# Kernel tuning notes

Measured on AMD Instinct MI355X. Metric: run time of the kernel, lower is better.

The kernel has to match this reference:

```python
import jax, jax.numpy as jnp
import numpy as np

NUM_HEADS = 16


def setup_inputs() -> dict:
    key = jax.random.key(0)
    ks = jax.random.split(key, 9)
    B, N, C, R, T = 16, 1024, 1024, 64, 10
    s = 0.02
    x = jax.random.normal(ks[0], (B, N, C), dtype=jnp.float32)
    W_qkv = jax.random.normal(ks[1], (3 * C, C), dtype=jnp.float32) * s
    W_proj = jax.random.normal(ks[2], (C, C), dtype=jnp.float32) * s
    b_proj = jax.random.normal(ks[3], (C,), dtype=jnp.float32) * s
    A_k = jax.random.normal(ks[4], (T, R, C), dtype=jnp.float32) * s
    B_k = jax.random.normal(ks[5], (T, C, R), dtype=jnp.float32) * s
    A_v = jax.random.normal(ks[6], (T, R, C), dtype=jnp.float32) * s
    B_v = jax.random.normal(ks[7], (T, C, R), dtype=jnp.float32) * s
    return {"x": x, "W_qkv": W_qkv, "W_proj": W_proj, "b_proj": b_proj,
            "A_k": A_k, "B_k": B_k, "A_v": A_v, "B_v": B_v, "task": 4}


def reference(x, W_qkv, W_proj, b_proj, A_k, B_k, A_v, B_v, task):
    B, N, C = x.shape
    H = NUM_HEADS
    hd = C // H
    scale = hd ** (-0.5)

    # qkv projection: x @ W_qkv.T -> [B,N,3C] -> [3,B,H,N,hd]
    qkv = (x @ W_qkv.T).reshape(B, N, 3, H, hd).transpose(2, 0, 3, 1, 4)
    q, k, v = qkv[0], qkv[1], qkv[2]

    # merged LoRA weights: sum_{t<=task} B[t] @ A[t] -> [C, C]
    w_k = jnp.einsum('tcr,trd->cd', B_k[:task + 1], A_k[:task + 1])
    w_v = jnp.einsum('tcr,trd->cd', B_v[:task + 1], A_v[:task + 1])
    # F.linear(x, W) = x @ W.T ; reshape to [B,H,N,hd]
    dk = (x @ w_k.T).reshape(B, N, H, hd).transpose(0, 2, 1, 3)
    dv = (x @ w_v.T).reshape(B, N, H, hd).transpose(0, 2, 1, 3)
    k = k + dk
    v = v + dv

    attn = jax.nn.softmax(jnp.einsum('bhnd,bhmd->bhnm', q, k) * scale, axis=-1)
    out = jnp.einsum('bhnm,bhmd->bhnd', attn, v)
    out = out.transpose(0, 2, 1, 3).reshape(B, N, C)
    return out @ W_proj.T + b_proj
```

## Files before the change

kernel.cpp:

```cpp
#include <hip/hip_runtime.h>

typedef __attribute__((ext_vector_type(4))) float f32x4;
typedef __attribute__((ext_vector_type(8))) short s16x8;
typedef __attribute__((ext_vector_type(2))) unsigned int u32x2;
typedef __attribute__((ext_vector_type(4))) unsigned int u32x4;

#define LOG2E 1.44269504088896340736f

__device__ inline unsigned short f2b(float f) {
  unsigned int u = __float_as_uint(f);
  unsigned int r = (u + 0x7FFFu + ((u >> 16) & 1u)) >> 16;
  return (unsigned short)r;
}

__device__ inline unsigned int cvtpk_bf16(float lo, float hi) {
  unsigned int r;
  asm("v_cvt_pk_bf16_f32 %0, %1, %2" : "=v"(r) : "v"(lo), "v"(hi));
  return r;
}

__device__ inline void gload_lds16(const unsigned short* g, unsigned short* l) {
  __builtin_amdgcn_global_load_lds(
      (const __attribute__((address_space(1))) unsigned int*)g,
      (__attribute__((address_space(3))) unsigned int*)l, 16, 0, 0);
}

__global__ __launch_bounds__(256) void lora_merge(const float* __restrict__ A_k,
                                                  const float* __restrict__ B_k,
                                                  const float* __restrict__ A_v,
                                                  const float* __restrict__ B_v,
                                                  float* __restrict__ wk,
                                                  float* __restrict__ wv,
                                                  const int* __restrict__ taskp) {
  const float* A_ = blockIdx.y ? A_v : A_k;
  const float* B_ = blockIdx.y ? B_v : B_k;
  float* Wd = blockIdx.y ? wv : wk;
  __shared__ float Bs[64][65];
  __shared__ float As[64][65];
  const int tile = blockIdx.x;
  const int c0 = (tile >> 4) * 64, d0 = (tile & 15) * 64;
  const int tid = threadIdx.x;
  const int tx = tid & 15, ty = tid >> 4;
  const int T = *taskp + 1;
  float acc[4][4] = {};
  const int r = tid >> 2, cb = (tid & 3) * 16;
  for (int t = 0; t < T; ++t) {
    __syncthreads();
    const float* srcB = B_ + (size_t)t * 65536 + (size_t)(c0 + r) * 64 + cb;
    const float* srcA = A_ + (size_t)t * 65536 + (size_t)r * 1024 + d0 + cb;
#pragma unroll
    for (int j = 0; j < 16; j += 4) {
      f32x4 vb = *(const f32x4*)(srcB + j);
      Bs[r][cb + j] = vb.x; Bs[r][cb + j + 1] = vb.y;
      Bs[r][cb + j + 2] = vb.z; Bs[r][cb + j + 3] = vb.w;
      f32x4 va = *(const f32x4*)(srcA + j);
      As[r][cb + j] = va.x; As[r][cb + j + 1] = va.y;
      As[r][cb + j + 2] = va.z; As[r][cb + j + 3] = va.w;
    }
    __syncthreads();
#pragma unroll 8
    for (int rr = 0; rr < 64; ++rr) {
      float bv[4], av[4];
#pragma unroll
      for (int i = 0; i < 4; ++i) bv[i] = Bs[ty * 4 + i][rr];
#pragma unroll
      for (int j = 0; j < 4; ++j) av[j] = As[rr][tx * 4 + j];
#pragma unroll
      for (int i = 0; i < 4; ++i)
#pragma unroll
        for (int j = 0; j < 4; ++j) acc[i][j] += bv[i] * av[j];
    }
  }
#pragma unroll
  for (int i = 0; i < 4; ++i)
#pragma unroll
    for (int j = 0; j < 4; ++j)
      Wd[(size_t)(c0 + ty * 4 + i) * 1024 + d0 + tx * 4 + j] = acc[i][j];
}

__global__ void prep_cvt(const float* __restrict__ x, const float* __restrict__ Wproj,
                         unsigned short* __restrict__ xb, unsigned short* __restrict__ Wp) {
  int i = blockIdx.x * 256 + threadIdx.x;
  const float* src;
  unsigned short* dst;
  int idx;
  if (i < 4194304) { src = x; dst = xb; idx = i; }
  else { idx = i - 4194304; if (idx >= 262144) return; src = Wproj; dst = Wp; }
  f32x4 v = ((const f32x4*)src)[idx];
  unsigned short o0 = f2b(v.x), o1 = f2b(v.y), o2 = f2b(v.z), o3 = f2b(v.w);
  unsigned long long pack = (unsigned long long)o0 | ((unsigned long long)o1 << 16) |
                            ((unsigned long long)o2 << 32) | ((unsigned long long)o3 << 48);
  ((unsigned long long*)dst)[idx] = pack;
}

__global__ void build_wc(const float* __restrict__ Wqkv, const float* __restrict__ wk,
                         const float* __restrict__ wv, unsigned short* __restrict__ Wc) {
  int i = blockIdx.x * 256 + threadIdx.x;
  int e = i * 4;
  f32x4 v = *(const f32x4*)(Wqkv + e);
  int row = e >> 10;
  if (row >= 2048) {
    f32x4 d = *(const f32x4*)(wv + (e - 2097152));
    v = v + d;
  } else if (row >= 1024) {
    f32x4 d = *(const f32x4*)(wk + (e - 1048576));
    v = v + d;
  }
  unsigned short o0 = f2b(v.x), o1 = f2b(v.y), o2 = f2b(v.z), o3 = f2b(v.w);
  unsigned long long pack = (unsigned long long)o0 | ((unsigned long long)o1 << 16) |
                            ((unsigned long long)o2 << 32) | ((unsigned long long)o3 << 48);
  ((unsigned long long*)Wc)[i] = pack;
}

template <int OUT_BF16, int ADD_BIAS>
__global__ __launch_bounds__(512, 1) void gemm256(const unsigned short* __restrict__ A,
                                                  const unsigned short* __restrict__ B,
                                                  void* __restrict__ Cout,
                                                  const float* __restrict__ bias,
                                                  int M, int N, int K) {
  __shared__ unsigned short SA[4][8192];
  __shared__ unsigned short SB[4][8192];
  const int tid = threadIdx.x;
  const int w = tid >> 6, l = tid & 63;
  const int lr = l & 15, lg = l >> 4;
  const int wm = w >> 2, wn = w & 3;

  const int lin = blockIdx.y * gridDim.x + blockIdx.x;
  const int cpx = (gridDim.x * gridDim.y) >> 3;
  const int s = (lin & 7) * cpx + (lin >> 3);
  const int bx = s % gridDim.x, by = s / gridDim.x;

  const int cs = tid ^ (((tid >> 5) & 1) << 1);
  const int r_st = ((cs >> 6) << 4) | ((cs >> 2) & 15);
  const int k_st = (cs & 3) << 3;
  const unsigned short* gA0 = A + (size_t)(by * 256 + r_st) * K + k_st;
  const unsigned short* gA1 = A + (size_t)(by * 256 + 128 + r_st) * K + k_st;
  const unsigned short* gB0 = B + (size_t)(bx * 256 + r_st) * K + k_st;
  const unsigned short* gB1 = B + (size_t)(bx * 256 + 128 + r_st) * K + k_st;
  const int wb = w * 512;

  const int swz = ((lr >> 3) & 1) << 4;
  const int fbase = lr * 32 + lg * 8;
  const int hA = wm * 4096;
  const int hB = (wn >> 1) * 4096;
  const int nb = (wn & 1) * 4;

  f32x4 acc[8][4] = {};
  const int NT = K >> 5;

#pragma unroll
  for (int t = 0; t < 3; ++t) {
    gload_lds16(gA0 + t * 32, &SA[t][wb]);
    gload_lds16(gA1 + t * 32, &SA[t][4096 + wb]);
    gload_lds16(gB0 + t * 32, &SB[t][wb]);
    gload_lds16(gB1 + t * 32, &SB[t][4096 + wb]);
  }
  asm volatile("s_waitcnt vmcnt(8)" ::: "memory");
  __builtin_amdgcn_s_barrier();
  __builtin_amdgcn_sched_barrier(0);

  for (int t = 0; t < NT; ++t) {
    const int slot = t & 3;
    const int ts = (t + 3 < NT) ? (t + 3) : (NT - 1);
    const int ssl = (t + 3) & 3;
    const unsigned short* sa = &SA[slot][hA];
    const unsigned short* sb = &SB[slot][hB];
    s16x8 af[8], bf[2];
#pragma unroll
    for (int m = 0; m < 8; ++m)
      af[m] = *(const s16x8*)&sa[(m * 512 + fbase) ^ swz];
#pragma unroll
    for (int n = 0; n < 2; ++n)
      bf[n] = *(const s16x8*)&sb[((nb + n) * 512 + fbase) ^ swz];
    gload_lds16(gA0 + ts * 32, &SA[ssl][wb]);
    gload_lds16(gA1 + ts * 32, &SA[ssl][4096 + wb]);
    __builtin_amdgcn_s_barrier();
    asm volatile("s_waitcnt lgkmcnt(0)" ::: "memory");
    __builtin_amdgcn_sched_barrier(0);
    __builtin_amdgcn_s_setprio(1);
#pragma unroll
    for (int m = 0; m < 8; ++m)
#pragma unroll
      for (int n = 0; n < 2; ++n)
        acc[m][n] = __builtin_amdgcn_mfma_f32_16x16x32_bf16(af[m], bf[n], acc[m][n], 0, 0, 0);
    __builtin_amdgcn_s_setprio(0);
    __builtin_amdgcn_sched_barrier(0);
    __builtin_amdgcn_s_barrier();
#pragma unroll
    for (int n = 0; n < 2; ++n)
      bf[n] = *(const s16x8*)&sb[((nb + 2 + n) * 512 + fbase) ^ swz];
    gload_lds16(gB0 + ts * 32, &SB[ssl][wb]);
    gload_lds16(gB1 + ts * 32, &SB[ssl][4096 + wb]);
    __builtin_amdgcn_s_barrier();
    asm volatile("s_waitcnt lgkmcnt(0)" ::: "memory");
    __builtin_amdgcn_sched_barrier(0);
    __builtin_amdgcn_s_setprio(1);
#pragma unroll
    for (int m = 0; m < 8; ++m)
#pragma unroll
      for (int n = 0; n < 2; ++n)
        acc[m][2 + n] = __builtin_amdgcn_mfma_f32_16x16x32_bf16(af[m], bf[n], acc[m][2 + n], 0, 0, 0);
    __builtin_amdgcn_s_setprio(0);
    __builtin_amdgcn_sched_barrier(0);
    asm volatile("s_waitcnt vmcnt(8)" ::: "memory");
    __builtin_amdgcn_s_barrier();
    __builtin_amdgcn_sched_barrier(0);
  }

  const int crow0 = by * 256 + wm * 128;
  const int ccol0 = bx * 256 + wn * 64;
  if (OUT_BF16) {
    unsigned short* C = (unsigned short*)Cout;
#pragma unroll
    for (int m = 0; m < 8; ++m)
#pragma unroll
      for (int n = 0; n < 4; ++n)
#pragma unroll
        for (int rr = 0; rr < 4; ++rr) {
          int row = crow0 + m * 16 + lg * 4 + rr;
          int col = ccol0 + n * 16 + lr;
          C[(size_t)row * N + col] = f2b(acc[m][n][rr]);
        }
  } else {
    float* C = (float*)Cout;
#pragma unroll
    for (int m = 0; m < 8; ++m)
#pragma unroll
      for (int n = 0; n < 4; ++n)
#pragma unroll
        for (int rr = 0; rr < 4; ++rr) {
          int row = crow0 + m * 16 + lg * 4 + rr;
          int col = ccol0 + n * 16 + lr;
          float b = ADD_BIAS ? bias[col] : 0.f;
          C[(size_t)row * N + col] = acc[m][n][rr] + b;
        }
  }
}

__global__ __launch_bounds__(64) void transpose_v(const unsigned short* __restrict__ qkv,
                                                  unsigned short* __restrict__ vT) {
  __shared__ unsigned short T[64 * 65];
  const int bh = blockIdx.x >> 4;
  const int nt = blockIdx.x & 15;
  const int b = bh >> 4, h = bh & 15;
  const int l = threadIdx.x;
  const unsigned short* src = qkv + (size_t)(b * 1024 + nt * 64) * 3072 + 2048 + h * 64;
#pragma unroll
  for (int p = 0; p < 8; ++p) {
    int slot = p * 64 + l;
    int n = slot >> 3, dc = (slot & 7) * 8;
    u32x4 v = *(const u32x4*)(src + (size_t)n * 3072 + dc);
    const unsigned short* vs = (const unsigned short*)&v;
#pragma unroll
    for (int j = 0; j < 8; ++j) T[n * 65 + dc + j] = vs[j];
  }
  __syncthreads();
  unsigned short* dst = vT + (size_t)bh * 65536 + nt * 64;
#pragma unroll
  for (int p = 0; p < 8; ++p) {
    int slot = p * 64 + l;
    int d = slot >> 3, nc = (slot & 7) * 8;
    union { unsigned short s[8]; u32x4 v; } tmp;
#pragma unroll
    for (int j = 0; j < 8; ++j) tmp.s[j] = T[(nc + j) * 65 + d];
    *(u32x4*)(dst + (size_t)d * 1024 + nc) = tmp.v;
  }
}

__global__ __launch_bounds__(512) void attn_fwd(const unsigned short* __restrict__ qkv,
                                                const unsigned short* __restrict__ vT,
                                                unsigned short* __restrict__ out) {
  const int tid = threadIdx.x;
  const int w = tid >> 6, l = tid & 63;
  const int lr = l & 15, lg = l >> 4;
  const int bid = blockIdx.x;
  const int g = (bid & 7) * 32 + (bid >> 5);
  const int qt2 = (bid >> 3) & 3;
  const int b = g >> 4, h = g & 15;

  __shared__ unsigned short Ks[2][4096];
  __shared__ unsigned short Vs[2][4096];
  __shared__ unsigned int Ps[16][576];

  const size_t base = (size_t)b * 1024 * 3072 + h * 64;
  const unsigned short* Qp = qkv + base;
  const unsigned short* Kp = qkv + base + 1024;
  const unsigned short* vTp = vT + (size_t)(b * 16 + h) * 65536;

  const float SSCALE = 0.125f * LOG2E;
  const int qb = qt2 * 256;
  s16x8 qf[2][2];
#pragma unroll
  for (int qg = 0; qg < 2; ++qg) {
    const int qrow = qb + qg * 128 + w * 16 + lr;
    qf[qg][0] = *(const s16x8*)(Qp + (size_t)qrow * 3072 + lg * 8);
    qf[qg][1] = *(const s16x8*)(Qp + (size_t)qrow * 3072 + 32 + lg * 8);
#pragma unroll
    for (int kk = 0; kk < 2; ++kk)
#pragma unroll
      for (int j = 0; j < 8; ++j) {
        float f = __uint_as_float(((unsigned int)(unsigned short)qf[qg][kk][j]) << 16) * SSCALE;
        qf[qg][kk][j] = (short)f2b(f);
      }
  }

  f32x4 o[2][4] = {};
  float lrun[2] = {0.f, 0.f};

  const int srow = tid >> 3;
  const int csrc = (tid & 7) ^ (srow & 7);

  gload_lds16(Kp + (size_t)srow * 3072 + csrc * 8, &Ks[0][w * 512]);
  gload_lds16(vTp + (size_t)srow * 1024 + csrc * 8, &Vs[0][w * 512]);
  __syncthreads();

  for (int t = 0; t < 16; ++t) {
    const int cur = t & 1;
    if (t < 15) {
      const int kv1 = (t + 1) * 64;
      gload_lds16(Kp + (size_t)(kv1 + srow) * 3072 + csrc * 8, &Ks[cur ^ 1][w * 512]);
      gload_lds16(vTp + (size_t)srow * 1024 + kv1 + csrc * 8, &Vs[cur ^ 1][w * 512]);
    }
    const unsigned short* Kb = &Ks[cur][0];
    const unsigned short* Vb = &Vs[cur][0];

#pragma unroll
    for (int qg = 0; qg < 2; ++qg) {
      unsigned int* Pw = &Ps[(w << 1) | qg][0];
      f32x4 sc[4];
#pragma unroll
      for (int tt = 0; tt < 4; ++tt) {
        f32x4 a = {0.f, 0.f, 0.f, 0.f};
#pragma unroll
        for (int kk = 0; kk < 2; ++kk) {
          int krow = tt * 16 + lr;
          s16x8 kf = *(const s16x8*)&Kb[krow * 64 + ((((kk * 32 + lg * 8) >> 3) ^ (krow & 7)) << 3)];
          a = __builtin_amdgcn_mfma_f32_16x16x32_bf16(kf, qf[qg][kk], a, 0, 0, 0);
        }
        sc[tt] = a;
      }

#pragma unroll
      for (int tt = 0; tt < 4; ++tt) {
        float p0 = exp2f(sc[tt][0]);
        float p1 = exp2f(sc[tt][1]);
        float p2 = exp2f(sc[tt][2]);
        float p3 = exp2f(sc[tt][3]);
        lrun[qg] += (p0 + p1) + (p2 + p3);
        u32x2 pk;
        pk.x = cvtpk_bf16(p0, p1);
        pk.y = cvtpk_bf16(p2, p3);
        *(u32x2*)&Pw[lr * 36 + tt * 8 + lg * 2] = pk;
      }
      __builtin_amdgcn_sched_barrier(0);

#pragma unroll
      for (int kk = 0; kk < 2; ++kk) {
        u32x4 pu = *(const u32x4*)&Pw[lr * 36 + kk * 16 + lg * 4];
        s16x8 pf = __builtin_bit_cast(s16x8, pu);
#pragma unroll
        for (int dt = 0; dt < 4; ++dt) {
          int vrow = dt * 16 + lr;
          s16x8 vf = *(const s16x8*)&Vb[vrow * 64 + ((((kk * 32 + lg * 8) >> 3) ^ (vrow & 7)) << 3)];
          o[qg][dt] = __builtin_amdgcn_mfma_f32_16x16x32_bf16(pf, vf, o[qg][dt], 0, 0, 0);
        }
      }
    }
    __syncthreads();
  }

#pragma unroll
  for (int qg = 0; qg < 2; ++qg) {
    float lr2 = lrun[qg];
    lr2 += __shfl_xor(lr2, 16);
    lr2 += __shfl_xor(lr2, 32);
    float lq[4];
#pragma unroll
    for (int rr = 0; rr < 4; ++rr) lq[rr] = 1.f / __shfl(lr2, lg * 4 + rr);
    const size_t orow0 = (size_t)b * 1024 + qb + qg * 128 + w * 16;
#pragma unroll
    for (int dt = 0; dt < 4; ++dt)
#pragma unroll
      for (int rr = 0; rr < 4; ++rr)
        out[(orow0 + lg * 4 + rr) * 1024 + h * 64 + dt * 16 + lr] = f2b(o[qg][dt][rr] * lq[rr]);
  }
}

extern "C" void kernel_launch(void* const* d_in, const int* in_sizes, int n_in,
                              void* d_out, int out_size, void* d_ws, size_t ws_size,
                              hipStream_t stream) {
  const float* x = (const float*)d_in[0];
  const float* Wqkv = (const float*)d_in[1];
  const float* Wproj = (const float*)d_in[2];
  const float* bproj = (const float*)d_in[3];
  const float* A_k = (const float*)d_in[4];
  const float* B_k = (const float*)d_in[5];
  const float* A_v = (const float*)d_in[6];
  const float* B_v = (const float*)d_in[7];
  const int* task = (const int*)d_in[8];

  char* ws = (char*)d_ws;
  float* wk = (float*)ws;
  float* wv = (float*)(ws + (4ull << 20));
  unsigned short* xb = (unsigned short*)(ws + (8ull << 20));
  unsigned short* Wc = (unsigned short*)(ws + (40ull << 20));
  unsigned short* Wp = (unsigned short*)(ws + (46ull << 20));
  unsigned short* qkv = (unsigned short*)(ws + (48ull << 20));
  unsigned short* ao = (unsigned short*)(ws + (144ull << 20));
  unsigned short* vT = xb;

  lora_merge<<<dim3(256, 2), 256, 0, stream>>>(A_k, B_k, A_v, B_v, wk, wv, task);
  prep_cvt<<<17408, 256, 0, stream>>>(x, Wproj, xb, Wp);
  build_wc<<<3072, 256, 0, stream>>>(Wqkv, wk, wv, Wc);
  gemm256<1, 0><<<dim3(12, 64), 512, 0, stream>>>(xb, Wc, qkv, nullptr, 16384, 3072, 1024);
  transpose_v<<<4096, 64, 0, stream>>>(qkv, vT);
  attn_fwd<<<1024, 512, 0, stream>>>(qkv, vT, ao);
  gemm256<0, 1><<<dim3(4, 64), 512, 0, stream>>>(ao, Wp, d_out, bproj, 16384, 1024, 1024);
}
```

Before: 341.3 us.

## Interleave both query groups' MFMAs and compute softmax row sums via MFMA with ones

The attention inner loop now computes QK^T scores for both query groups together and shares each K fragment load between them. It writes both P tiles before a single PV phase that also shares V fragment loads. The running softmax denominator no longer comes from VALU adds and shuffles; it is accumulated by an extra MFMA of P against a vector of bf16 ones, which sums the bf16-rounded probabilities. s_setprio hints are added around MFMA blocks to favour matrix issue. The cost is more live registers for the doubled score accumulators, plus two extra MFMAs per kk step.

```diff
diff --git a/kernel.cpp b/kernel.cpp
--- a/kernel.cpp
+++ b/kernel.cpp
@@ -304,8 +304,12 @@
       }
   }
 
+  s16x8 ONES;
+#pragma unroll
+  for (int j = 0; j < 8; ++j) ONES[j] = (short)0x3F80;
+
   f32x4 o[2][4] = {};
-  float lrun[2] = {0.f, 0.f};
+  f32x4 o4[2] = {};
 
   const int srow = tid >> 3;
   const int csrc = (tid & 7) ^ (srow & 7);
@@ -324,59 +328,62 @@
     const unsigned short* Kb = &Ks[cur][0];
     const unsigned short* Vb = &Vs[cur][0];
 
+    f32x4 sc[2][4] = {};
+    __builtin_amdgcn_s_setprio(1);
+#pragma unroll
+    for (int kk = 0; kk < 2; ++kk)
+#pragma unroll
+      for (int tt = 0; tt < 4; ++tt) {
+        int krow = tt * 16 + lr;
+        s16x8 kf = *(const s16x8*)&Kb[krow * 64 + ((((kk * 32 + lg * 8) >> 3) ^ (krow & 7)) << 3)];
+        sc[0][tt] = __builtin_amdgcn_mfma_f32_16x16x32_bf16(kf, qf[0][kk], sc[0][tt], 0, 0, 0);
+        sc[1][tt] = __builtin_amdgcn_mfma_f32_16x16x32_bf16(kf, qf[1][kk], sc[1][tt], 0, 0, 0);
+      }
+    __builtin_amdgcn_s_setprio(0);
+
 #pragma unroll
     for (int qg = 0; qg < 2; ++qg) {
       unsigned int* Pw = &Ps[(w << 1) | qg][0];
-      f32x4 sc[4];
 #pragma unroll
       for (int tt = 0; tt < 4; ++tt) {
-        f32x4 a = {0.f, 0.f, 0.f, 0.f};
-#pragma unroll
-        for (int kk = 0; kk < 2; ++kk) {
-          int krow = tt * 16 + lr;
-          s16x8 kf = *(const s16x8*)&Kb[krow * 64 + ((((kk * 32 + lg * 8) >> 3) ^ (krow & 7)) << 3)];
-          a = __builtin_amdgcn_mfma_f32_16x16x32_bf16(kf, qf[qg][kk], a, 0, 0, 0);
-        }
-        sc[tt] = a;
-      }
-
-#pragma unroll
-      for (int tt = 0; tt < 4; ++tt) {
-        float p0 = exp2f(sc[tt][0]);
-        float p1 = exp2f(sc[tt][1]);
-        float p2 = exp2f(sc[tt][2]);
-        float p3 = exp2f(sc[tt][3]);
-        lrun[qg] += (p0 + p1) + (p2 + p3);
+        float p0 = exp2f(sc[qg][tt][0]);
+        float p1 = exp2f(sc[qg][tt][1]);
+        float p2 = exp2f(sc[qg][tt][2]);
+        float p3 = exp2f(sc[qg][tt][3]);
         u32x2 pk;
         pk.x = cvtpk_bf16(p0, p1);
         pk.y = cvtpk_bf16(p2, p3);
         *(u32x2*)&Pw[lr * 36 + tt * 8 + lg * 2] = pk;
       }
-      __builtin_amdgcn_sched_barrier(0);
-
-#pragma unroll
-      for (int kk = 0; kk < 2; ++kk) {
-        u32x4 pu = *(const u32x4*)&Pw[lr * 36 + kk * 16 + lg * 4];
-        s16x8 pf = __builtin_bit_cast(s16x8, pu);
-#pragma unroll
-        for (int dt = 0; dt < 4; ++dt) {
-          int vrow = dt * 16 + lr;
-          s16x8 vf = *(const s16x8*)&Vb[vrow * 64 + ((((kk * 32 + lg * 8) >> 3) ^ (vrow & 7)) << 3)];
-          o[qg][dt] = __builtin_amdgcn_mfma_f32_16x16x32_bf16(pf, vf, o[qg][dt], 0, 0, 0);
-        }
+    }
+    __builtin_amdgcn_sched_barrier(0);
+
+#pragma unroll
+    for (int kk = 0; kk < 2; ++kk) {
+      u32x4 pu0 = *(const u32x4*)&Ps[(w << 1)][lr * 36 + kk * 16 + lg * 4];
+      u32x4 pu1 = *(const u32x4*)&Ps[(w << 1) | 1][lr * 36 + kk * 16 + lg * 4];
+      s16x8 pf0 = __builtin_bit_cast(s16x8, pu0);
+      s16x8 pf1 = __builtin_bit_cast(s16x8, pu1);
+      __builtin_amdgcn_s_setprio(1);
+      o4[0] = __builtin_amdgcn_mfma_f32_16x16x32_bf16(pf0, ONES, o4[0], 0, 0, 0);
+      o4[1] = __builtin_amdgcn_mfma_f32_16x16x32_bf16(pf1, ONES, o4[1], 0, 0, 0);
+#pragma unroll
+      for (int dt = 0; dt < 4; ++dt) {
+        int vrow = dt * 16 + lr;
+        s16x8 vf = *(const s16x8*)&Vb[vrow * 64 + ((((kk * 32 + lg * 8) >> 3) ^ (vrow & 7)) << 3)];
+        o[0][dt] = __builtin_amdgcn_mfma_f32_16x16x32_bf16(pf0, vf, o[0][dt], 0, 0, 0);
+        o[1][dt] = __builtin_amdgcn_mfma_f32_16x16x32_bf16(pf1, vf, o[1][dt], 0, 0, 0);
       }
+      __builtin_amdgcn_s_setprio(0);
     }
     __syncthreads();
   }
 
 #pragma unroll
   for (int qg = 0; qg < 2; ++qg) {
-    float lr2 = lrun[qg];
-    lr2 += __shfl_xor(lr2, 16);
-    lr2 += __shfl_xor(lr2, 32);
-    float lq[4];
-#pragma unroll
-    for (int rr = 0; rr < 4; ++rr) lq[rr] = 1.f / __shfl(lr2, lg * 4 + rr);
+    f32x4 lq;
+#pragma unroll
+    for (int rr = 0; rr < 4; ++rr) lq[rr] = 1.f / o4[qg][rr];
     const size_t orow0 = (size_t)b * 1024 + qb + qg * 128 + w * 16;
 #pragma unroll
     for (int dt = 0; dt < 4; ++dt)
```

Result: faster. 331.1 us (-3.0%).
